# Kernel tuning notes

Measured on AMD Instinct MI355X. Metric: run time of the kernel, lower is better.

## Reference

```python
import math
import jax, jax.numpy as jnp
import numpy as np

B, T, E, H = 2, 1024, 1024, 16
D = E // H            # head dim
NREL = 529            # local-relation vocab (max_ary=32)
KMAX = 32             # rel_kmax
RVOC = 64             # tree relation vocab
SQRT = 3.0            # args.sqrt
INF = 10000000000.0
EPS = 1e-06


def _layernorm(x, w, b):
    # TF-style: divide by (std + eps), std is unbiased (torch default ddof=1)
    u = jnp.mean(x, axis=-1, keepdims=True)
    s = jnp.std(x - u, axis=-1, ddof=1, keepdims=True)
    return w * (x - u) / (s + EPS) + b


def _gelu(x):
    return 0.5 * x * (1.0 + jnp.tanh(math.sqrt(2.0 / math.pi) * (x + 0.044715 * x ** 3)))


def setup_inputs() -> dict:
    key = jax.random.key(0)
    ks = jax.random.split(key, 24)
    f32 = jnp.float32
    inp = {
        'x': jax.random.normal(ks[0], (B, T, E), f32),
        'tds': 0.1 * jax.random.normal(ks[1], (B, H, T, T), f32),
        'LR_Q': 0.1 * jax.random.normal(ks[2], (H, NREL, D), f32),
        'LR_K': 0.1 * jax.random.normal(ks[3], (H, NREL, D), f32),
        'rel': jax.random.randint(ks[4], (B, T, T), 0, RVOC, jnp.int32),
        'LR_map': jax.random.randint(ks[5], (B, T, T), 0, NREL, jnp.int32),
        # parameters (Linear weights stored as [in, out])
        'Wqkv': 0.02 * jax.random.normal(ks[6], (E, 3 * E), f32),
        'bqkv': jnp.zeros((3 * E,), f32),
        'Wproj': 0.02 * jax.random.normal(ks[7], (E, E), f32),
        'bproj': jnp.zeros((E,), f32),
        'rel_weights': 1.0 + 0.02 * jax.random.normal(ks[8], (RVOC, H), f32),
        'rel_keys': 0.02 * jax.random.normal(ks[9], (2 * KMAX + 1, D), f32),
        'rel_values': 0.02 * jax.random.normal(ks[10], (2 * KMAX + 1, D), f32),
        'ln1_w': jnp.ones((E,), f32), 'ln1_b': jnp.zeros((E,), f32),
        'ln2_w': jnp.ones((E,), f32), 'ln2_b': jnp.zeros((E,), f32),
        'Wfc': 0.02 * jax.random.normal(ks[11], (E, 4 * E), f32),
        'bfc': jnp.zeros((4 * E,), f32),
        'Wfp': 0.02 * jax.random.normal(ks[12], (4 * E, E), f32),
        'bfp': jnp.zeros((E,), f32),
    }
    return inp


def reference(x, tds, LR_Q, LR_K, Wqkv, bqkv, Wproj, bproj, rel_weights,
              rel_keys, rel_values, ln1_w, ln1_b, ln2_w, ln2_b,
              Wfc, bfc, Wfp, bfp, rel, LR_map):
    inv_sqrt_d = 1.0 / math.sqrt(D)
    # --- attention branch ---
    h = _layernorm(x, ln1_w, ln1_b)
    qkv = h @ Wqkv + bqkv                                   # [B,T,3E]
    q, k, v = jnp.split(qkv, 3, axis=-1)
    q = q.reshape(B, T, H, D).transpose(0, 2, 1, 3)         # [B,H,T,D]
    k = k.reshape(B, T, H, D).transpose(0, 2, 1, 3)
    v = v.reshape(B, T, H, D).transpose(0, 2, 1, 3)

    w = jnp.einsum('bhid,bhjd->bhij', q, k)                 # raw scores
    # sequential relative keys (rel_ids buffer)
    idx = jnp.arange(T)
    rel_ids = jnp.clip(idx[None, :] - idx[:, None], -KMAX, KMAX) + KMAX  # [T,T]
    relk = rel_keys[rel_ids]                                # [T,T,D]
    w = w + jnp.einsum('bhid,ijd->bhij', q, relk)
    w = w * inv_sqrt_d                                      # self.scale

    bmask = jnp.tril(jnp.ones((T, T), jnp.float32))         # causal bias buffer
    # tree relation (multiplicative, additive=False)
    rele = rel_weights[rel].transpose(0, 3, 1, 2)           # [B,H,T,T]
    w = w * (rele * bmask)
    # TD tree positional encoding
    w = w + tds
    # local relation terms with gather
    lmap = jnp.broadcast_to(LR_map[:, None], (B, H, T, T))
    lr1 = jnp.einsum('bhid,hnd->bhin', q, LR_K) * inv_sqrt_d  # [B,H,T,N]
    lr1 = jnp.take_along_axis(lr1, lmap, axis=-1)             # [B,H,T,T]
    lr2 = jnp.einsum('hnd,bhjd->bhnj', LR_Q, k) * inv_sqrt_d  # [B,H,N,T]
    lr2 = jnp.take_along_axis(lr2, lmap, axis=-2)             # [B,H,T,T]
    w = (w + lr1 + lr2) / math.sqrt(SQRT)

    w = w * bmask - INF * (1.0 - bmask)
    p = jax.nn.softmax(w, axis=-1)
    ret = jnp.einsum('bhij,bhjd->bhid', p, v)
    relv = rel_values[rel_ids]                               # [T,T,D]
    ret = ret + jnp.einsum('bhij,ijd->bhid', p, relv)
    a = ret.transpose(0, 2, 1, 3).reshape(B, T, E) @ Wproj + bproj
    x = x + a
    # --- MLP branch ---
    h2 = _layernorm(x, ln2_w, ln2_b)
    m = _gelu(h2 @ Wfc + bfc) @ Wfp + bfp
    return x + m
```

## Files before the change

### kernel.cpp

```cpp
#include <hip/hip_runtime.h>
#include <hip/hip_bf16.h>
#include <math.h>

typedef __hip_bfloat16 bf16;
typedef __attribute__((ext_vector_type(8))) short short8;
typedef __attribute__((ext_vector_type(4))) float f32x4;

#define B_    2
#define T_    1024
#define E_    1024
#define H_    16
#define NREL_ 529
#define E3_   3072
#define E4_   4096

#define AS1 __attribute__((address_space(1)))
#define AS3 __attribute__((address_space(3)))

__device__ __forceinline__ void gload16(const void* g, void* l) {
  __builtin_amdgcn_global_load_lds((const AS1 unsigned int*)g,
                                   (AS3 unsigned int*)l, 16, 0, 0);
}
__device__ __forceinline__ float b2f(short s) {
  union { unsigned u; float f; } c; c.u = ((unsigned)(unsigned short)s) << 16; return c.f;
}
__device__ __forceinline__ float ldmix(const void* p, size_t i, int isbf) {
  return isbf ? b2f(((const short*)p)[i]) : ((const float*)p)[i];
}
__device__ __forceinline__ void stmix(void* p, size_t i, int isbf, float v) {
  if (isbf) ((bf16*)p)[i] = __float2bfloat16(v);
  else      ((float*)p)[i] = v;
}
__device__ __forceinline__ float waveReduceSum(float v) {
#pragma unroll
  for (int o = 32; o > 0; o >>= 1) v += __shfl_xor(v, o);
  return v;
}

__global__ void probe_kernel(const unsigned* __restrict__ w, int* __restrict__ flag) {
  if (threadIdx.x == 0 && blockIdx.x == 0) *flag = (w[0] == 0x3F803F80u) ? 1 : 0;
}

__global__ __launch_bounds__(256) void ln_kernel(const void* __restrict__ x,
    const void* __restrict__ w, const void* __restrict__ bia, bf16* __restrict__ out,
    const int* __restrict__ flag, int xIsBf) {
  __shared__ float scr[4];
  int isbf = *flag;
  int xbf = isbf | xIsBf;
  int row = blockIdx.x, t = threadIdx.x;
  size_t base = (size_t)row * E_;
  float v[4]; float sum = 0.f;
#pragma unroll
  for (int u = 0; u < 4; u++) { v[u] = ldmix(x, base + u * 256 + t, xbf); sum += v[u]; }
  sum = waveReduceSum(sum);
  if ((t & 63) == 0) scr[t >> 6] = sum;
  __syncthreads();
  sum = scr[0] + scr[1] + scr[2] + scr[3];
  float mean = sum * (1.f / E_);
  float ss = 0.f;
#pragma unroll
  for (int u = 0; u < 4; u++) { float d = v[u] - mean; ss += d * d; }
  ss = waveReduceSum(ss);
  __syncthreads();
  if ((t & 63) == 0) scr[t >> 6] = ss;
  __syncthreads();
  ss = scr[0] + scr[1] + scr[2] + scr[3];
  float istd = 1.f / (sqrtf(ss * (1.f / (E_ - 1))) + 1e-6f);
#pragma unroll
  for (int u = 0; u < 4; u++) {
    int c = u * 256 + t;
    out[base + c] = __float2bfloat16(ldmix(w, c, isbf) * (v[u] - mean) * istd
                                     + ldmix(bia, c, isbf));
  }
}

__global__ __launch_bounds__(256) void tconv_kernel(const void* __restrict__ W,
    bf16* __restrict__ Wt, int K, int N, const int* __restrict__ flag) {
  __shared__ float tile[32][33];
  int isbf = *flag;
  int k0 = blockIdx.x * 32, n0 = blockIdx.y * 32;
  int t = threadIdx.x, c = t & 31, r0 = t >> 5;
#pragma unroll
  for (int rr = 0; rr < 4; rr++) {
    int r = r0 + rr * 8;
    tile[r][c] = ldmix(W, (size_t)(k0 + r) * N + n0 + c, isbf);
  }
  __syncthreads();
#pragma unroll
  for (int rr = 0; rr < 4; rr++) {
    int r = r0 + rr * 8;
    Wt[(size_t)(n0 + r) * K + k0 + c] = __float2bfloat16(tile[c][r]);
  }
}

__global__ __launch_bounds__(256) void vt_kernel(const bf16* __restrict__ qkv,
    bf16* __restrict__ vT) {
  __shared__ short tile[32][33];
  int j0 = blockIdx.x * 32, d0 = blockIdx.y * 32;
  int bh = blockIdx.z; int b = bh >> 4, h = bh & 15;
  int t = threadIdx.x, c = t & 31, r0 = t >> 5;
#pragma unroll
  for (int rr = 0; rr < 4; rr++) {
    int r = r0 + rr * 8;
    tile[r][c] = ((const short*)qkv)[(size_t)(b * T_ + j0 + r) * E3_ + 2 * E_ + h * 64 + d0 + c];
  }
  __syncthreads();
#pragma unroll
  for (int rr = 0; rr < 4; rr++) {
    int r = r0 + rr * 8;
    ((short*)vT)[((size_t)(b * H_ + h) * 64 + d0 + r) * T_ + j0 + c] = tile[c][r];
  }
}

__global__ __launch_bounds__(256) void prep_kernel(const void* __restrict__ relk,
    const void* __restrict__ relv, bf16* __restrict__ relkB, bf16* __restrict__ relvT,
    const int* __restrict__ flag) {
  int isbf = *flag, t = threadIdx.x;
  for (int i = t; i < 48 * 64; i += 256) {
    int tt = i >> 6, d = i & 63;
    relkB[i] = __float2bfloat16(tt < 33 ? ldmix(relk, (size_t)tt * 64 + d, isbf) : 0.f);
  }
  for (int i = t; i < 64 * 64; i += 256) {
    int d = i >> 6, tt = i & 63;
    relvT[i] = __float2bfloat16(tt < 33 ? ldmix(relv, (size_t)tt * 64 + d, isbf) : 0.f);
  }
}

__global__ __launch_bounds__(256) void padlr_kernel(const void* __restrict__ LR,
    bf16* __restrict__ LRp, const int* __restrict__ flag) {
  int isbf = *flag;
  int h = blockIdx.y, t = threadIdx.x;
  int n = blockIdx.x * 4 + (t >> 6), d = t & 63;
  float v = (n < NREL_) ? ldmix(LR, ((size_t)h * NREL_ + n) * 64 + d, isbf) : 0.f;
  LRp[((size_t)h * 640 + n) * 64 + d] = __float2bfloat16(v);
}

template <int BN>
__device__ void mgemm_body(const bf16* __restrict__ A, int lda,
    const bf16* __restrict__ Wt, const void* __restrict__ bias,
    const void* __restrict__ resid, void* __restrict__ C, int ldc,
    int K, int nmax, int act, int outbf, int resbf, float cscale,
    int bm, int bn, int isbf) {
  __shared__ __align__(16) short As[128 * 64];
  __shared__ __align__(16) short Bs[BN * 64];
  constexpr int MI = (BN == 128) ? 4 : 2;
  int t = threadIdx.x, w = t >> 6, lane = t & 63;
  int wm = (BN == 128) ? (w & 1) * 64 : w * 32;
  int wn = (BN == 128) ? (w >> 1) * 64 : 0;
  int cg = ((lane & 7) ^ ((lane >> 3) & 7)) * 8;
  int rsub = lane >> 3;
  int bw = (BN == 128) ? w * 32 : (w & 1) * 32;
  const bf16* gA = A  + (size_t)(bm + w * 32 + rsub) * lda + cg;
  const bf16* gB = Wt + (size_t)(bn + bw + rsub) * K + cg;
  short* lA = As + (w * 32) * 64;
  short* lB = Bs + bw * 64;
  f32x4 acc[MI][4] = {};
  int lm = lane & 15, kq = lane >> 4;
  for (int k0 = 0; k0 < K; k0 += 64) {
#pragma unroll
    for (int i = 0; i < 4; i++)
      gload16(gA + (size_t)i * 8 * lda + k0, lA + i * 8 * 64);
    if (BN == 128 || w < 2) {
#pragma unroll
      for (int i = 0; i < 4; i++)
        gload16(gB + (size_t)i * 8 * K + k0, lB + i * 8 * 64);
    }
    __syncthreads();
#pragma unroll
    for (int ks = 0; ks < 2; ks++) {
      short8 af[MI], bf_[4];
#pragma unroll
      for (int mi = 0; mi < MI; mi++) {
        int row = wm + mi * 16 + lm;
        int ci = (ks * 4 + kq) ^ (lm & 7);
        af[mi] = *(const short8*)&As[row * 64 + ci * 8];
      }
#pragma unroll
      for (int ni = 0; ni < 4; ni++) {
        int row = wn + ni * 16 + lm;
        int ci = (ks * 4 + kq) ^ (lm & 7);
        bf_[ni] = *(const short8*)&Bs[row * 64 + ci * 8];
      }
#pragma unroll
      for (int mi = 0; mi < MI; mi++)
#pragma unroll
        for (int ni = 0; ni < 4; ni++)
          acc[mi][ni] = __builtin_amdgcn_mfma_f32_16x16x32_bf16(
              af[mi], bf_[ni], acc[mi][ni], 0, 0, 0);
    }
    __syncthreads();
  }
  int rq = lane >> 4;
#pragma unroll
  for (int ni = 0; ni < 4; ni++) {
    int col = bn + wn + ni * 16 + lm;
    if (col < nmax) {
      float bv = bias ? ldmix(bias, col, isbf) : 0.f;
#pragma unroll
      for (int mi = 0; mi < MI; mi++) {
#pragma unroll
        for (int r = 0; r < 4; r++) {
          int rowg = bm + wm + mi * 16 + rq * 4 + r;
          float v = acc[mi][ni][r] * cscale + bv;
          if (act == 1) {
            float uu = 0.7978845608028654f * (v + 0.044715f * v * v * v);
            v = v / (1.f + __expf(-2.f * uu));
          }
          size_t off = (size_t)rowg * ldc + col;
          if (resid) v += ldmix(resid, off, resbf);
          stmix(C, off, outbf, v);
        }
      }
    }
  }
}

__global__ __launch_bounds__(256) void mgemm_kernel(const bf16* __restrict__ A,
    const bf16* __restrict__ Wt, const void* __restrict__ bias,
    const void* __restrict__ resid, void* __restrict__ C,
    int N, int K, int act, int mode, const int* __restrict__ flag) {
  int isbf = *flag;
  int outbf = (mode == 1) ? isbf : 1;
  int resbf = (mode == 1) ? 1 : isbf;
  mgemm_body<128>(A, K, Wt, bias, resid, C, N, K, N, act, outbf, resbf, 1.f,
                  blockIdx.y * 128, blockIdx.x * 128, isbf);
}

__global__ __launch_bounds__(256) void mgemm64_kernel(const bf16* __restrict__ A,
    const bf16* __restrict__ Wt, const void* __restrict__ bias,
    const void* __restrict__ resid, void* __restrict__ C,
    int N, int K, int act, int mode, const int* __restrict__ flag) {
  int isbf = *flag;
  int outbf = (mode == 1) ? isbf : 1;
  int resbf = (mode == 1) ? 1 : isbf;
  mgemm_body<64>(A, K, Wt, bias, resid, C, N, K, N, act, outbf, resbf, 1.f,
                 blockIdx.y * 128, blockIdx.x * 64, isbf);
}

__global__ __launch_bounds__(256) void lrmm_kernel(const bf16* __restrict__ qkv,
    const bf16* __restrict__ LRp, bf16* __restrict__ out, int koff, int b0) {
  int z = blockIdx.z, h = z & 15, b = b0 + (z >> 4);
  const bf16* A = qkv + (size_t)(b * T_) * E3_ + h * 64 + koff;
  const bf16* Wt = LRp + (size_t)h * 640 * 64;
  bf16* C = out + (size_t)z * T_ * NREL_;
  mgemm_body<128>(A, E3_, Wt, nullptr, nullptr, C, NREL_, 64, NREL_, 0, 1, 1, 0.125f,
                  blockIdx.y * 128, blockIdx.x * 128, 0);
}

#define MF(a, b, c) __builtin_amdgcn_mfma_f32_16x16x32_bf16(a, b, c, 0, 0, 0)

#define LOADIDX(J0X, RA, MA, TDA) do { \
  _Pragma("unroll") for (int nt2 = 0; nt2 < 2; nt2++) { \
    _Pragma("unroll") for (int r2 = 0; r2 < 4; r2++) { \
      int e2 = nt2 * 4 + r2; \
      int jj = (J0X) + nt2 * 16 + col; \
      int ii = i0 + q * 4 + r2; \
      RA[e2] = 0; MA[e2] = 0; TDA[e2] = 0.f; \
      if (jj <= ii) { \
        size_t oo = (size_t)ii * T_ + jj; \
        RA[e2] = rel0[oo]; MA[e2] = map0[oo]; \
        TDA[e2] = ldmix(tds, tdsbase + oo, isbf); \
      } } } \
} while (0)

#define GATHVAL(J0X, RA, MA, WA, V1A, V2A) do { \
  _Pragma("unroll") for (int nt2 = 0; nt2 < 2; nt2++) { \
    _Pragma("unroll") for (int r2 = 0; r2 < 4; r2++) { \
      int e2 = nt2 * 4 + r2; \
      int jj = (J0X) + nt2 * 16 + col; \
      int ii = i0 + q * 4 + r2; \
      WA[e2] = sW[RA[e2]]; \
      V1A[e2] = b2f(sL1[(q * 4 + r2) * NREL_ + MA[e2]]); \
      V2A[e2] = 0.f; \
      if (jj <= ii) V2A[e2] = b2f(lr2h[(size_t)jj * NREL_ + MA[e2]]); \
    } } \
} while (0)

__global__ __launch_bounds__(64, 2) void attn_kernel(const bf16* __restrict__ qkv,
    const void* __restrict__ tds, const void* __restrict__ relw,
    const int* __restrict__ rel, const int* __restrict__ lmap,
    const bf16* __restrict__ lr1, const bf16* __restrict__ lr2,
    const bf16* __restrict__ vT, const bf16* __restrict__ relkB,
    const bf16* __restrict__ relvT, bf16* __restrict__ retE,
    int b0, const int* __restrict__ flag) {
  __shared__ __align__(16) short sQ[16 * 64];
  __shared__ __align__(16) short sK[32 * 64];
  __shared__ __align__(16) short sVt[64 * 32];
  __shared__ __align__(16) short sP[16 * 40];
  __shared__ __align__(16) short sPb[16 * 72];
  __shared__ __align__(16) short sL1[8704];
  __shared__ float qrkT[16 * 36];
  __shared__ float sW[64];
  __shared__ float mT[16], lT[16];

  int isbf = *flag;
  int lane = threadIdx.x;
  int h = blockIdx.x;
  int zz = blockIdx.y;
  int b = b0 + blockIdx.z;
  int col = lane & 15, q = lane >> 4;

  const short* kbase = (const short*)qkv + (size_t)b * T_ * E3_ + E_ + h * 64;
  const short* vtb   = (const short*)vT + ((size_t)(b * H_ + h) * 64) * T_;
  const int* rel0  = rel  + (size_t)b * T_ * T_;
  const int* map0  = lmap + (size_t)b * T_ * T_;
  size_t tdsbase = ((size_t)(b * H_ + h) * T_) * T_;
  const short* lr1h = (const short*)lr1 + (size_t)(blockIdx.z * H_ + h) * T_ * NREL_;
  const short* lr2h = (const short*)lr2 + (size_t)(blockIdx.z * H_ + h) * T_ * NREL_;

  sW[lane] = ldmix(relw, (size_t)lane * H_ + h, isbf);

  for (int half = 0; half < 2; half++) {
    int it = half ? (63 - zz) : zz;
    int i0 = it * 16;
    int ntile = ((i0 + 15) >> 5) + 1;

    {
      int r = lane >> 3, c = lane & 7;
#pragma unroll
      for (int i = 0; i < 2; i++) {
        int row = i * 8 + r;
        gload16((const short*)qkv + (size_t)(b * T_ + i0 + row) * E3_ + h * 64
                + ((c ^ (row & 7)) * 8), sQ + i * 8 * 64);
      }
      const short* l1src = lr1h + (size_t)i0 * NREL_;
#pragma unroll
      for (int k2 = 0; k2 < 17; k2++)
        gload16(l1src + (size_t)(k2 * 64 + lane) * 8, sL1 + k2 * 64 * 8);
    }
    __builtin_amdgcn_s_waitcnt(0x0F70);
    short8 qf[2];
#pragma unroll
    for (int ko = 0; ko < 2; ko++)
      qf[ko] = *(const short8*)&sQ[col * 64 + (((ko * 4 + q) ^ (col & 7)) * 8)];

#pragma unroll
    for (int nt = 0; nt < 3; nt++) {
      f32x4 z = {};
      const short* rp = (const short*)relkB + (size_t)(nt * 16 + col) * 64 + q * 8;
      z = MF(qf[0], *(const short8*)rp, z);
      z = MF(qf[1], *(const short8*)(rp + 32), z);
      int t = nt * 16 + col;
      if (t < 33) {
#pragma unroll
        for (int r = 0; r < 4; r++) qrkT[(q * 4 + r) * 36 + t] = z[r];
      }
    }

    f32x4 acc[4] = {};
    float m_r[4], l_r[4];
#pragma unroll
    for (int r = 0; r < 4; r++) { m_r[r] = -3e38f; l_r[r] = 0.f; }

    int r8 = lane >> 3, c8 = lane & 7;
    int r4 = lane >> 2, c4 = lane & 3;
    short8 kreg[4], vreg[4];
    int nrel[8], nmap[8]; float ntds[8];
    int trel[8], tmap[8]; float ttds[8];
    float cw[8], c1[8], c2[8], ctds[8];
    float nw[8], n1[8], n2[8];

    LOADIDX(0, nrel, nmap, ntds);
#pragma unroll
    for (int i = 0; i < 4; i++) {
      int row = i * 8 + r8;
      kreg[i] = *(const short8*)(kbase + (size_t)row * E3_ + ((c8 ^ (row & 7)) * 8));
    }
#pragma unroll
    for (int i = 0; i < 4; i++) {
      int row = i * 16 + r4;
      vreg[i] = *(const short8*)(vtb + (size_t)row * T_ + ((c4 ^ (row & 3)) * 8));
    }
    GATHVAL(0, nrel, nmap, cw, c1, c2);
#pragma unroll
    for (int e = 0; e < 8; e++) ctds[e] = ntds[e];
    if (ntile > 1) LOADIDX(32, nrel, nmap, ntds);
#pragma unroll
    for (int i = 0; i < 4; i++) {
      int row = i * 8 + r8;
      *(short8*)&sK[row * 64 + c8 * 8] = kreg[i];
    }
#pragma unroll
    for (int i = 0; i < 4; i++) {
      int row = i * 16 + r4;
      *(short8*)&sVt[row * 32 + c4 * 8] = vreg[i];
    }

    for (int jt = 0; jt < ntile; jt++) {
      int j0 = jt * 32;
      int more = (jt + 1 < ntile);
      if (more) {
        int j0n = j0 + 32;
#pragma unroll
        for (int i = 0; i < 4; i++) {
          int row = i * 8 + r8;
          kreg[i] = *(const short8*)(kbase + (size_t)(j0n + row) * E3_
                                     + ((c8 ^ (row & 7)) * 8));
        }
#pragma unroll
        for (int i = 0; i < 4; i++) {
          int row = i * 16 + r4;
          vreg[i] = *(const short8*)(vtb + (size_t)row * T_ + j0n
                                     + ((c4 ^ (row & 3)) * 8));
        }
        GATHVAL(j0n, nrel, nmap, nw, n1, n2);
        if (jt + 2 < ntile) LOADIDX(j0 + 64, trel, tmap, ttds);
      }

      f32x4 sA[2];
#pragma unroll
      for (int nt = 0; nt < 2; nt++) {
        f32x4 z = {};
#pragma unroll
        for (int ko = 0; ko < 2; ko++) {
          short8 kf = *(const short8*)&sK[(nt * 16 + col) * 64
                                          + (((ko * 4 + q) ^ (col & 7)) * 8)];
          z = MF(qf[ko], kf, z);
        }
        sA[nt] = z;
      }
      float sv[2][4];
#pragma unroll
      for (int nt = 0; nt < 2; nt++) {
        int j = j0 + nt * 16 + col;
#pragma unroll
        for (int r = 0; r < 4; r++) {
          int i = i0 + q * 4 + r;
          int e = nt * 4 + r;
          float x = -1e10f;
          if (j <= i) {
            int rid = j - i + 32; rid = rid < 0 ? 0 : rid;
            float s1 = (sA[nt][r] + qrkT[(q * 4 + r) * 36 + rid]) * 0.125f;
            s1 = s1 * cw[e] + ctds[e];
            s1 = (s1 + c1[e] + c2[e]) * 0.57735026918962576f;
            x = s1;
          }
          sv[nt][r] = x;
        }
      }
#pragma unroll
      for (int r = 0; r < 4; r++) {
        float tm = fmaxf(sv[0][r], sv[1][r]);
#pragma unroll
        for (int o = 1; o < 16; o <<= 1) tm = fmaxf(tm, __shfl_xor(tm, o));
        float mn = fmaxf(m_r[r], tm);
        float al = __expf(m_r[r] - mn);
        m_r[r] = mn;
#pragma unroll
        for (int dt = 0; dt < 4; dt++) acc[dt][r] *= al;
        float p0 = __expf(sv[0][r] - mn), p1 = __expf(sv[1][r] - mn);
        float rs = p0 + p1;
#pragma unroll
        for (int o = 1; o < 16; o <<= 1) rs += __shfl_xor(rs, o);
        l_r[r] = l_r[r] * al + rs;
        ((bf16*)sP)[(q * 4 + r) * 40 + col]      = __float2bfloat16(p0);
        ((bf16*)sP)[(q * 4 + r) * 40 + 16 + col] = __float2bfloat16(p1);
      }
      short8 pf = *(const short8*)&sP[col * 40 + q * 8];
#pragma unroll
      for (int dt = 0; dt < 4; dt++) {
        int row = dt * 16 + col;
        short8 vf = *(const short8*)&sVt[row * 32 + ((q ^ (row & 3)) * 8)];
        acc[dt] = MF(pf, vf, acc[dt]);
      }

      if (more) {
#pragma unroll
        for (int i = 0; i < 4; i++) {
          int row = i * 8 + r8;
          *(short8*)&sK[row * 64 + c8 * 8] = kreg[i];
        }
#pragma unroll
        for (int i = 0; i < 4; i++) {
          int row = i * 16 + r4;
          *(short8*)&sVt[row * 32 + c4 * 8] = vreg[i];
        }
#pragma unroll
        for (int e = 0; e < 8; e++) {
          cw[e] = nw[e]; c1[e] = n1[e]; c2[e] = n2[e]; ctds[e] = ntds[e];
        }
        if (jt + 2 < ntile) {
#pragma unroll
          for (int e = 0; e < 8; e++) {
            nrel[e] = trel[e]; nmap[e] = tmap[e]; ntds[e] = ttds[e];
          }
        }
      }
    }

#pragma unroll
    for (int r = 0; r < 4; r++) {
      float inv = 1.f / l_r[r];
#pragma unroll
      for (int dt = 0; dt < 4; dt++) acc[dt][r] *= inv;
    }
    if (col == 0) {
#pragma unroll
      for (int r = 0; r < 4; r++) { mT[q * 4 + r] = m_r[r]; lT[q * 4 + r] = l_r[r]; }
    }
    for (int k2 = lane; k2 < 16 * 36; k2 += 64) ((unsigned*)sPb)[k2] = 0u;
    int brow = col, ig = i0 + brow;
    short8 qv[8];
#pragma unroll
    for (int c2 = 0; c2 < 8; c2++)
      qv[c2] = *(const short8*)&sQ[brow * 64 + ((c2 ^ (brow & 7)) * 8)];
    float mfin = mT[brow], lfin = lT[brow];
    float sump = 0.f;
#pragma unroll
    for (int e = 0; e < 8; e++) {
      int tt = q * 8 + e + 1;
      int j = ig + tt - 32;
      if (j >= 0) {
        const short* kj = kbase + (size_t)j * E3_;
        float dacc = 0.f;
#pragma unroll
        for (int c2 = 0; c2 < 8; c2++) {
          short8 kk = *(const short8*)(kj + c2 * 8);
          short8 qq = qv[c2];
#pragma unroll
          for (int e2 = 0; e2 < 8; e2++) dacc += b2f(qq[e2]) * b2f(kk[e2]);
        }
        float s1 = (dacc + qrkT[brow * 36 + tt]) * 0.125f;
        s1 *= sW[rel0[(size_t)ig * T_ + j]];
        s1 += ldmix(tds, tdsbase + (size_t)ig * T_ + j, isbf);
        int mm = map0[(size_t)ig * T_ + j];
        s1 = (s1 + b2f(sL1[brow * NREL_ + mm])
                 + b2f(lr2h[(size_t)j * NREL_ + mm])) * 0.57735026918962576f;
        float pn = __expf(s1 - mfin) / lfin;
        ((bf16*)sPb)[brow * 72 + tt] = __float2bfloat16(pn);
        sump += pn;
      }
    }
    sump += __shfl_xor(sump, 16); sump += __shfl_xor(sump, 32);
    if (q == 0) ((bf16*)sPb)[brow * 72] = __float2bfloat16(fmaxf(1.f - sump, 0.f));
    short8 pbf[2];
#pragma unroll
    for (int ko = 0; ko < 2; ko++)
      pbf[ko] = *(const short8*)&sPb[col * 72 + ko * 32 + q * 8];
#pragma unroll
    for (int dt = 0; dt < 4; dt++) {
#pragma unroll
      for (int ko = 0; ko < 2; ko++) {
        int row = dt * 16 + col;
        short8 rv = *(const short8*)((const short*)relvT + (size_t)row * 64
                                     + (ko * 4 + q) * 8);
        acc[dt] = MF(pbf[ko], rv, acc[dt]);
      }
    }
#pragma unroll
    for (int dt = 0; dt < 4; dt++)
#pragma unroll
      for (int r = 0; r < 4; r++)
        retE[(size_t)(b * T_ + i0 + q * 4 + r) * E_ + h * 64 + dt * 16 + col]
            = __float2bfloat16(acc[dt][r]);
  }
}

extern "C" void kernel_launch(void* const* d_in, const int* in_sizes, int n_in,
                              void* d_out, int out_size, void* d_ws, size_t ws_size,
                              hipStream_t stream) {
  (void)in_sizes; (void)n_in; (void)out_size;
  const void* x    = d_in[0];
  const void* tds  = d_in[1];
  const void* LRQ  = d_in[2];
  const void* LRK  = d_in[3];
  const int*  rel  = (const int*)d_in[4];
  const int*  lmap = (const int*)d_in[5];
  const void* Wqkv = d_in[6];
  const void* bqkv = d_in[7];
  const void* Wproj= d_in[8];
  const void* bproj= d_in[9];
  const void* relw = d_in[10];
  const void* relk = d_in[11];
  const void* relv = d_in[12];
  const void* ln1w = d_in[13];
  const void* ln1b = d_in[14];
  const void* ln2w = d_in[15];
  const void* ln2b = d_in[16];
  const void* Wfc  = d_in[17];
  const void* bfc  = d_in[18];
  const void* Wfp  = d_in[19];
  const void* bfp  = d_in[20];

  char* wsp = (char*)d_ws;
  bf16* qkv   = (bf16*)(wsp + 0);
  bf16* WfcT  = (bf16*)(wsp + 0);
  bf16* h     = (bf16*)(wsp + 12582912);
  bf16* LRKp  = (bf16*)(wsp + 12582912);
  bf16* LRQp  = (bf16*)(wsp + 13893632);
  bf16* x2    = (bf16*)(wsp + 12582912);
  bf16* WqkvT = (bf16*)(wsp + 16777216);
  bf16* lr1p  = (bf16*)(wsp + 16777216);
  bf16* WfpT  = (bf16*)(wsp + 16777216);
  bf16* lr2p  = (bf16*)(wsp + 34111488);
  bf16* WprojT= (bf16*)(wsp + 34111488);
  bf16* g     = (bf16*)(wsp + 34111488);
  bf16* retE  = (bf16*)(wsp + 51445760);
  bf16* h2    = (bf16*)(wsp + 51445760);
  int*  flag  = (int*) (wsp + 55640064);
  bf16* vT    = (bf16*)(wsp + 55640320);
  bf16* relkB = (bf16*)(wsp + 59834624);
  bf16* relvT = (bf16*)(wsp + 59840768);
  bf16* lr2d  = (bf16*)(wsp + 59848960);
  bool dual = ws_size >= 94517504u;

  probe_kernel<<<1, 64, 0, stream>>>((const unsigned*)ln1w, flag);
  prep_kernel<<<1, 256, 0, stream>>>(relk, relv, relkB, relvT, flag);

  tconv_kernel<<<dim3(E_ / 32, E3_ / 32), 256, 0, stream>>>(Wqkv, WqkvT, E_, E3_, flag);
  ln_kernel<<<B_ * T_, 256, 0, stream>>>(x, ln1w, ln1b, h, flag, 0);
  mgemm_kernel<<<dim3(E3_ / 128, (B_ * T_) / 128), 256, 0, stream>>>(
      h, WqkvT, bqkv, nullptr, qkv, E3_, E_, 0, 0, flag);
  vt_kernel<<<dim3(T_ / 32, 2, B_ * H_), 256, 0, stream>>>(qkv, vT);
  padlr_kernel<<<dim3(160, H_), 256, 0, stream>>>(LRK, LRKp, flag);
  padlr_kernel<<<dim3(160, H_), 256, 0, stream>>>(LRQ, LRQp, flag);

  if (dual) {
    lrmm_kernel<<<dim3(5, 8, 32), 256, 0, stream>>>(qkv, LRKp, lr1p, 0, 0);
    lrmm_kernel<<<dim3(5, 8, 32), 256, 0, stream>>>(qkv, LRQp, lr2d, E_, 0);
    attn_kernel<<<dim3(H_, 32, B_), 64, 0, stream>>>(qkv, tds, relw, rel, lmap,
        lr1p, lr2d, vT, relkB, relvT, retE, 0, flag);
  } else {
    for (int b = 0; b < B_; b++) {
      lrmm_kernel<<<dim3(5, 8, 16), 256, 0, stream>>>(qkv, LRKp, lr1p, 0, b);
      lrmm_kernel<<<dim3(5, 8, 16), 256, 0, stream>>>(qkv, LRQp, lr2p, E_, b);
      attn_kernel<<<dim3(H_, 32, 1), 64, 0, stream>>>(qkv, tds, relw, rel, lmap,
          lr1p, lr2p, vT, relkB, relvT, retE, b, flag);
    }
  }

  tconv_kernel<<<dim3(E_ / 32, E_ / 32), 256, 0, stream>>>(Wproj, WprojT, E_, E_, flag);
  tconv_kernel<<<dim3(E_ / 32, E4_ / 32), 256, 0, stream>>>(Wfc, WfcT, E_, E4_, flag);
  tconv_kernel<<<dim3(E4_ / 32, E_ / 32), 256, 0, stream>>>(Wfp, WfpT, E4_, E_, flag);

  mgemm64_kernel<<<dim3(E_ / 64, (B_ * T_) / 128), 256, 0, stream>>>(
      retE, WprojT, bproj, x, x2, E_, E_, 0, 0, flag);
  ln_kernel<<<B_ * T_, 256, 0, stream>>>(x2, ln2w, ln2b, h2, flag, 1);
  mgemm_kernel<<<dim3(E4_ / 128, (B_ * T_) / 128), 256, 0, stream>>>(
      h2, WfcT, bfc, nullptr, g, E4_, E_, 1, 0, flag);
  mgemm64_kernel<<<dim3(E_ / 64, (B_ * T_) / 128), 256, 0, stream>>>(
      g, WfpT, bfp, x2, d_out, E_, E4_, 0, 1, flag);
}
```

Measured before the change: 750.1 us.

## Split attention key tiles across two waves with flash-style merge

```diff
diff --git a/kernel.cpp b/kernel.cpp
--- a/kernel.cpp
+++ b/kernel.cpp
@@ -276,7 +276,7 @@
     } } \
 } while (0)
 
-__global__ __launch_bounds__(64, 2) void attn_kernel(const bf16* __restrict__ qkv,
+__global__ __launch_bounds__(128, 2) void attn_kernel(const bf16* __restrict__ qkv,
     const void* __restrict__ tds, const void* __restrict__ relw,
     const int* __restrict__ rel, const int* __restrict__ lmap,
     const bf16* __restrict__ lr1, const bf16* __restrict__ lr2,
@@ -284,17 +284,16 @@
     const bf16* __restrict__ relvT, bf16* __restrict__ retE,
     int b0, const int* __restrict__ flag) {
   __shared__ __align__(16) short sQ[16 * 64];
-  __shared__ __align__(16) short sK[32 * 64];
-  __shared__ __align__(16) short sVt[64 * 32];
-  __shared__ __align__(16) short sP[16 * 40];
-  __shared__ __align__(16) short sPb[16 * 72];
+  __shared__ __align__(16) short sK2[2][32 * 64];
+  __shared__ __align__(16) short sPu[1280];
   __shared__ __align__(16) short sL1[8704];
   __shared__ float qrkT[16 * 36];
   __shared__ float sW[64];
-  __shared__ float mT[16], lT[16];
+  __shared__ float mrgM[2][16], mrgL[2][16], mrgS[2][16];
+  __shared__ float MM[16], LL[16];
 
   int isbf = *flag;
-  int lane = threadIdx.x;
+  int tid = threadIdx.x, w = tid >> 6, lane = tid & 63;
   int h = blockIdx.x;
   int zz = blockIdx.y;
   int b = b0 + blockIdx.z;
@@ -308,44 +307,60 @@
   const short* lr1h = (const short*)lr1 + (size_t)(blockIdx.z * H_ + h) * T_ * NREL_;
   const short* lr2h = (const short*)lr2 + (size_t)(blockIdx.z * H_ + h) * T_ * NREL_;
 
-  sW[lane] = ldmix(relw, (size_t)lane * H_ + h, isbf);
+  if (tid < 64) sW[tid] = ldmix(relw, (size_t)tid * H_ + h, isbf);
+
+  short* sK = sK2[w];
+  short* sP = sPu + w * 640;
+  short* sPb = sPu;
 
   for (int half = 0; half < 2; half++) {
     int it = half ? (63 - zz) : zz;
     int i0 = it * 16;
     int ntile = ((i0 + 15) >> 5) + 1;
 
+    __syncthreads();
     {
       int r = lane >> 3, c = lane & 7;
-#pragma unroll
-      for (int i = 0; i < 2; i++) {
-        int row = i * 8 + r;
-        gload16((const short*)qkv + (size_t)(b * T_ + i0 + row) * E3_ + h * 64
-                + ((c ^ (row & 7)) * 8), sQ + i * 8 * 64);
-      }
       const short* l1src = lr1h + (size_t)i0 * NREL_;
-#pragma unroll
-      for (int k2 = 0; k2 < 17; k2++)
-        gload16(l1src + (size_t)(k2 * 64 + lane) * 8, sL1 + k2 * 64 * 8);
+      if (w == 0) {
+#pragma unroll
+        for (int i = 0; i < 2; i++) {
+          int row = i * 8 + r;
+          gload16((const short*)qkv + (size_t)(b * T_ + i0 + row) * E3_ + h * 64
+                  + ((c ^ (row & 7)) * 8), sQ + i * 8 * 64);
+        }
+#pragma unroll
+        for (int k2 = 0; k2 < 8; k2++)
+          gload16(l1src + (size_t)(k2 * 64 + lane) * 8, sL1 + k2 * 512);
+      } else {
+#pragma unroll
+        for (int k2 = 8; k2 < 17; k2++)
+          gload16(l1src + (size_t)(k2 * 64 + lane) * 8, sL1 + k2 * 512);
+      }
     }
     __builtin_amdgcn_s_waitcnt(0x0F70);
+    __syncthreads();
+
     short8 qf[2];
 #pragma unroll
     for (int ko = 0; ko < 2; ko++)
       qf[ko] = *(const short8*)&sQ[col * 64 + (((ko * 4 + q) ^ (col & 7)) * 8)];
 
-#pragma unroll
-    for (int nt = 0; nt < 3; nt++) {
-      f32x4 z = {};
-      const short* rp = (const short*)relkB + (size_t)(nt * 16 + col) * 64 + q * 8;
-      z = MF(qf[0], *(const short8*)rp, z);
-      z = MF(qf[1], *(const short8*)(rp + 32), z);
-      int t = nt * 16 + col;
-      if (t < 33) {
-#pragma unroll
-        for (int r = 0; r < 4; r++) qrkT[(q * 4 + r) * 36 + t] = z[r];
-      }
-    }
+    if (w == 0) {
+#pragma unroll
+      for (int nt = 0; nt < 3; nt++) {
+        f32x4 z = {};
+        const short* rp = (const short*)relkB + (size_t)(nt * 16 + col) * 64 + q * 8;
+        z = MF(qf[0], *(const short8*)rp, z);
+        z = MF(qf[1], *(const short8*)(rp + 32), z);
+        int t = nt * 16 + col;
+        if (t < 33) {
+#pragma unroll
+          for (int r = 0; r < 4; r++) qrkT[(q * 4 + r) * 36 + t] = z[r];
+        }
+      }
+    }
+    __syncthreads();
 
     f32x4 acc[4] = {};
     float m_r[4], l_r[4];
@@ -353,58 +368,49 @@
     for (int r = 0; r < 4; r++) { m_r[r] = -3e38f; l_r[r] = 0.f; }
 
     int r8 = lane >> 3, c8 = lane & 7;
-    int r4 = lane >> 2, c4 = lane & 3;
-    short8 kreg[4], vreg[4];
+    short8 kreg[4];
     int nrel[8], nmap[8]; float ntds[8];
     int trel[8], tmap[8]; float ttds[8];
     float cw[8], c1[8], c2[8], ctds[8];
     float nw[8], n1[8], n2[8];
 
-    LOADIDX(0, nrel, nmap, ntds);
-#pragma unroll
-    for (int i = 0; i < 4; i++) {
-      int row = i * 8 + r8;
-      kreg[i] = *(const short8*)(kbase + (size_t)row * E3_ + ((c8 ^ (row & 7)) * 8));
-    }
-#pragma unroll
-    for (int i = 0; i < 4; i++) {
-      int row = i * 16 + r4;
-      vreg[i] = *(const short8*)(vtb + (size_t)row * T_ + ((c4 ^ (row & 3)) * 8));
-    }
-    GATHVAL(0, nrel, nmap, cw, c1, c2);
-#pragma unroll
-    for (int e = 0; e < 8; e++) ctds[e] = ntds[e];
-    if (ntile > 1) LOADIDX(32, nrel, nmap, ntds);
-#pragma unroll
-    for (int i = 0; i < 4; i++) {
-      int row = i * 8 + r8;
-      *(short8*)&sK[row * 64 + c8 * 8] = kreg[i];
-    }
-#pragma unroll
-    for (int i = 0; i < 4; i++) {
-      int row = i * 16 + r4;
-      *(short8*)&sVt[row * 32 + c4 * 8] = vreg[i];
-    }
-
-    for (int jt = 0; jt < ntile; jt++) {
+    if (w < ntile) {
+      int j00 = w * 32;
+      LOADIDX(j00, nrel, nmap, ntds);
+#pragma unroll
+      for (int i = 0; i < 4; i++) {
+        int row = i * 8 + r8;
+        kreg[i] = *(const short8*)(kbase + (size_t)(j00 + row) * E3_
+                                   + ((c8 ^ (row & 7)) * 8));
+      }
+      GATHVAL(j00, nrel, nmap, cw, c1, c2);
+#pragma unroll
+      for (int e = 0; e < 8; e++) ctds[e] = ntds[e];
+      if (w + 2 < ntile) LOADIDX(j00 + 64, nrel, nmap, ntds);
+#pragma unroll
+      for (int i = 0; i < 4; i++) {
+        int row = i * 8 + r8;
+        *(short8*)&sK[row * 64 + c8 * 8] = kreg[i];
+      }
+    }
+
+    for (int jt = w; jt < ntile; jt += 2) {
       int j0 = jt * 32;
-      int more = (jt + 1 < ntile);
+      int more = (jt + 2 < ntile);
+      short8 vf[4];
+#pragma unroll
+      for (int dt = 0; dt < 4; dt++)
+        vf[dt] = *(const short8*)(vtb + (size_t)(dt * 16 + col) * T_ + j0 + q * 8);
       if (more) {
-        int j0n = j0 + 32;
+        int j0n = j0 + 64;
 #pragma unroll
         for (int i = 0; i < 4; i++) {
           int row = i * 8 + r8;
           kreg[i] = *(const short8*)(kbase + (size_t)(j0n + row) * E3_
                                      + ((c8 ^ (row & 7)) * 8));
         }
-#pragma unroll
-        for (int i = 0; i < 4; i++) {
-          int row = i * 16 + r4;
-          vreg[i] = *(const short8*)(vtb + (size_t)row * T_ + j0n
-                                     + ((c4 ^ (row & 3)) * 8));
-        }
         GATHVAL(j0n, nrel, nmap, nw, n1, n2);
-        if (jt + 2 < ntile) LOADIDX(j0 + 64, trel, tmap, ttds);
+        if (jt + 4 < ntile) LOADIDX(j0 + 128, trel, tmap, ttds);
       }
 
       f32x4 sA[2];
@@ -458,11 +464,7 @@
       }
       short8 pf = *(const short8*)&sP[col * 40 + q * 8];
 #pragma unroll
-      for (int dt = 0; dt < 4; dt++) {
-        int row = dt * 16 + col;
-        short8 vf = *(const short8*)&sVt[row * 32 + ((q ^ (row & 3)) * 8)];
-        acc[dt] = MF(pf, vf, acc[dt]);
-      }
+      for (int dt = 0; dt < 4; dt++) acc[dt] = MF(pf, vf[dt], acc[dt]);
 
       if (more) {
 #pragma unroll
@@ -471,15 +473,10 @@
           *(short8*)&sK[row * 64 + c8 * 8] = kreg[i];
         }
 #pragma unroll
-        for (int i = 0; i < 4; i++) {
-          int row = i * 16 + r4;
-          *(short8*)&sVt[row * 32 + c4 * 8] = vreg[i];
-        }
-#pragma unroll
         for (int e = 0; e < 8; e++) {
           cw[e] = nw[e]; c1[e] = n1[e]; c2[e] = n2[e]; ctds[e] = ntds[e];
         }
-        if (jt + 2 < ntile) {
+        if (jt + 4 < ntile) {
 #pragma unroll
           for (int e = 0; e < 8; e++) {
             nrel[e] = trel[e]; nmap[e] = tmap[e]; ntds[e] = ttds[e];
@@ -488,27 +485,65 @@
       }
     }
 
+    if (col == 0) {
+#pragma unroll
+      for (int r = 0; r < 4; r++) {
+        mrgM[w][q * 4 + r] = m_r[r];
+        mrgL[w][q * 4 + r] = l_r[r];
+      }
+    }
+    __syncthreads();
+    float fw_[4];
 #pragma unroll
     for (int r = 0; r < 4; r++) {
-      float inv = 1.f / l_r[r];
-#pragma unroll
-      for (int dt = 0; dt < 4; dt++) acc[dt][r] *= inv;
-    }
-    if (col == 0) {
-#pragma unroll
-      for (int r = 0; r < 4; r++) { mT[q * 4 + r] = m_r[r]; lT[q * 4 + r] = l_r[r]; }
-    }
-    for (int k2 = lane; k2 < 16 * 36; k2 += 64) ((unsigned*)sPb)[k2] = 0u;
+      int row = q * 4 + r;
+      float M = fmaxf(mrgM[0][row], mrgM[1][row]);
+      fw_[r] = __expf(m_r[r] - M);
+      if (w == 0 && col == 0) {
+        MM[row] = M;
+        LL[row] = mrgL[0][row] * __expf(mrgM[0][row] - M)
+                + mrgL[1][row] * __expf(mrgM[1][row] - M);
+      }
+    }
+#pragma unroll
+    for (int dt = 0; dt < 4; dt++)
+#pragma unroll
+      for (int r = 0; r < 4; r++) acc[dt][r] *= fw_[r];
+    float* accX = (float*)sK2;
+    if (w == 1) {
+#pragma unroll
+      for (int dt = 0; dt < 4; dt++)
+#pragma unroll
+        for (int r = 0; r < 4; r++)
+          accX[(q * 4 + r) * 64 + dt * 16 + col] = acc[dt][r];
+    }
+    __syncthreads();
+    if (w == 0) {
+#pragma unroll
+      for (int dt = 0; dt < 4; dt++)
+#pragma unroll
+        for (int r = 0; r < 4; r++)
+          acc[dt][r] += accX[(q * 4 + r) * 64 + dt * 16 + col];
+#pragma unroll
+      for (int r = 0; r < 4; r++) {
+        float inv = 1.f / LL[q * 4 + r];
+#pragma unroll
+        for (int dt = 0; dt < 4; dt++) acc[dt][r] *= inv;
+      }
+    }
+    for (int k2 = tid; k2 < 576; k2 += 128) ((unsigned*)sPb)[k2] = 0u;
+    __syncthreads();
+
     int brow = col, ig = i0 + brow;
     short8 qv[8];
 #pragma unroll
     for (int c2 = 0; c2 < 8; c2++)
       qv[c2] = *(const short8*)&sQ[brow * 64 + ((c2 ^ (brow & 7)) * 8)];
-    float mfin = mT[brow], lfin = lT[brow];
+    float mfin = MM[brow], lfin = LL[brow];
     float sump = 0.f;
 #pragma unroll
-    for (int e = 0; e < 8; e++) {
-      int tt = q * 8 + e + 1;
+    for (int e = 0; e < 4; e++) {
+      int tt = q * 8 + w * 4 + e + 1;
       int j = ig + tt - 32;
       if (j >= 0) {
         const short* kj = kbase + (size_t)j * E3_;
@@ -532,27 +567,34 @@
       }
     }
     sump += __shfl_xor(sump, 16); sump += __shfl_xor(sump, 32);
-    if (q == 0) ((bf16*)sPb)[brow * 72] = __float2bfloat16(fmaxf(1.f - sump, 0.f));
-    short8 pbf[2];
-#pragma unroll
-    for (int ko = 0; ko < 2; ko++)
-      pbf[ko] = *(const short8*)&sPb[col * 72 + ko * 32 + q * 8];
-#pragma unroll
-    for (int dt = 0; dt < 4; dt++) {
-#pragma unroll
-      for (int ko = 0; ko < 2; ko++) {
-        int row = dt * 16 + col;
-        short8 rv = *(const short8*)((const short*)relvT + (size_t)row * 64
-                                     + (ko * 4 + q) * 8);
-        acc[dt] = MF(pbf[ko], rv, acc[dt]);
-      }
-    }
-#pragma unroll
-    for (int dt = 0; dt < 4; dt++)
-#pragma unroll
-      for (int r = 0; r < 4; r++)
-        retE[(size_t)(b * T_ + i0 + q * 4 + r) * E_ + h * 64 + dt * 16 + col]
-            = __float2bfloat16(acc[dt][r]);
+    if (q == 0) mrgS[w][brow] = sump;
+    __syncthreads();
+    if (w == 0 && q == 0)
+      ((bf16*)sPb)[brow * 72] = __float2bfloat16(
+          fmaxf(1.f - mrgS[0][brow] - mrgS[1][brow], 0.f));
+    __syncthreads();
+    if (w == 0) {
+      short8 pbf[2];
+#pragma unroll
+      for (int ko = 0; ko < 2; ko++)
+        pbf[ko] = *(const short8*)&sPb[col * 72 + ko * 32 + q * 8];
+#pragma unroll
+      for (int dt = 0; dt < 4; dt++) {
+#pragma unroll
+        for (int ko = 0; ko < 2; ko++) {
+          int row = dt * 16 + col;
+          short8 rv = *(const short8*)((const short*)relvT + (size_t)row * 64
+                                       + (ko * 4 + q) * 8);
+          acc[dt] = MF(pbf[ko], rv, acc[dt]);
+        }
+      }
+#pragma unroll
+      for (int dt = 0; dt < 4; dt++)
+#pragma unroll
+        for (int r = 0; r < 4; r++)
+          retE[(size_t)(b * T_ + i0 + q * 4 + r) * E_ + h * 64 + dt * 16 + col]
+              = __float2bfloat16(acc[dt][r]);
+    }
   }
 }
 
@@ -618,13 +660,13 @@
   if (dual) {
     lrmm_kernel<<<dim3(5, 8, 32), 256, 0, stream>>>(qkv, LRKp, lr1p, 0, 0);
     lrmm_kernel<<<dim3(5, 8, 32), 256, 0, stream>>>(qkv, LRQp, lr2d, E_, 0);
-    attn_kernel<<<dim3(H_, 32, B_), 64, 0, stream>>>(qkv, tds, relw, rel, lmap,
+    attn_kernel<<<dim3(H_, 32, B_), 128, 0, stream>>>(qkv, tds, relw, rel, lmap,
         lr1p, lr2d, vT, relkB, relvT, retE, 0, flag);
   } else {
     for (int b = 0; b < B_; b++) {
       lrmm_kernel<<<dim3(5, 8, 16), 256, 0, stream>>>(qkv, LRKp, lr1p, 0, b);
       lrmm_kernel<<<dim3(5, 8, 16), 256, 0, stream>>>(qkv, LRQp, lr2p, E_, b);
-      attn_kernel<<<dim3(H_, 32, 1), 64, 0, stream>>>(qkv, tds, relw, rel, lmap,
+      attn_kernel<<<dim3(H_, 32, 1), 128, 0, stream>>>(qkv, tds, relw, rel, lmap,
           lr1p, lr2p, vT, relkB, relvT, retE, b, flag);
     }
   }
```

New measurement: 733.6 us. -2.2%, faster.
